# Optimization experiments

Hardware: AMD Instinct MI355X
Metric: run time of the kernel (lower is better)

The kernel has to match this reference:

```python
import jax, jax.numpy as jnp
import numpy as np
from jax import lax

# Lens/aperture geometry (must match init_kwargs lens_mask)
LENS = 21
RADIUS = LENS // 2
EPS = 1e-8


def _offsets():
    """Flattened 21x21 aperture footprint: distance kernel, circular lens mask,
    and (row, col) slice offsets into the padded image."""
    ys, xs = np.meshgrid(np.arange(LENS), np.arange(LENS), indexing='ij')
    dy = ys - RADIUS
    dx = xs - RADIUS
    dist = np.sqrt(dy * dy + dx * dx).astype(np.float32)
    mask = (dist <= RADIUS).astype(np.float32)
    return (jnp.asarray(dist.ravel()), jnp.asarray(mask.ravel()),
            jnp.asarray(ys.ravel().astype(np.int32)),
            jnp.asarray(xs.ravel().astype(np.int32)))


def scatter_layer(x5, lens_effect):
    """Scatter (splat) defocus rendering of one RGBAD layer.

    x5: [B,5,H,W] (r,g,b,alpha,relative-disparity); lens_effect: [B,1].
    Each source pixel splats its premultiplied color over a disk of radius
    r = |disp| * lens_effect (soft-edged, area-normalized). Because the disk
    kernel is symmetric in the offset, the scatter is computed as a gather
    over the 21x21 footprint with weights taken from the *source* pixel.

    Returns [B,5,H,W]: [:3] accumulated rgb, [3] accumulated weight,
    [4] occupancy (clipped accumulated alpha-weight).
    """
    B, _, H, W = x5.shape
    dist, mask, oy, ox = _offsets()
    rgb, a, disp = x5[:, :3], x5[:, 3:4], x5[:, 4:5]
    r = jnp.clip(jnp.abs(disp) * lens_effect[:, :, None, None], 0.0, float(RADIUS))  # [B,1,H,W]

    # per-source-pixel soft disk area: sum_o mask(o) * clip(r + 0.5 - dist(o), 0, 1)
    def area_step(acc, dm):
        d, m = dm
        return acc + m * jnp.clip(r + 0.5 - d, 0.0, 1.0), None

    area, _ = lax.scan(area_step, jnp.zeros_like(r), (dist, mask))

    # premultiplied source energy, normalized by splat area
    s = jnp.concatenate([rgb * a, a], axis=1) / (area + EPS)  # [B,4,H,W]
    pad = ((0, 0), (0, 0), (RADIUS, RADIUS), (RADIUS, RADIUS))
    s_pad = jnp.pad(s, pad)
    r_pad = jnp.pad(r, pad)

    # gather formulation of the scatter: out[q] = sum_o s[q-o] * w(o; r[q-o])
    def step(acc, dmyx):
        d, m, dy, dx = dmyx
        sl = lax.dynamic_slice(s_pad, (0, 0, dy, dx), (B, 4, H, W))
        rsl = lax.dynamic_slice(r_pad, (0, 0, dy, dx), (B, 1, H, W))
        w = m * jnp.clip(rsl + 0.5 - d, 0.0, 1.0)
        return acc + sl * w, None

    out4, _ = lax.scan(step, jnp.zeros((B, 4, H, W), x5.dtype), (dist, mask, oy, ox))
    occu = jnp.clip(out4[:, 3:4], 0.0, 1.0)
    return jnp.concatenate([out4, occu], axis=1)


def setup_inputs() -> dict:
    key = jax.random.key(0)
    k1, k2 = jax.random.split(key)
    B, N_LAYER, H, W = 2, 3, 512, 512
    rgbad_layers = jax.random.uniform(k1, (B, 5 * N_LAYER, H, W), dtype=jnp.float32)
    # lens strength in a range that exercises the full 21x21 footprint
    lens_effect = jax.random.uniform(k2, (B, 1), dtype=jnp.float32) * 10.0
    focal = jnp.zeros((B, 5 * N_LAYER, H, W), dtype=jnp.float32)
    return {"rgbad_layers": rgbad_layers, "lens_effect": lens_effect, "focal": focal}


def reference(rgbad_layers, lens_effect, focal):
    """Multi_Layer_Renderer.forward: front-to-back alpha compositing of
    per-layer scatter-rendered bokeh."""
    x = rgbad_layers - focal
    n_layer = x.shape[1] // 5
    blurs = [scatter_layer(x[:, 5 * i:5 * (i + 1)], lens_effect) for i in range(n_layer)]
    rgb0, w0, o0 = blurs[0][:, :3], blurs[0][:, 3:4], blurs[0][:, 4:5]
    blur_rgb = rgb0 / (w0 + EPS) * o0
    trans = 1.0 - o0  # accumulated transmittance
    for li in range(1, n_layer):
        lr, lw, lo = blurs[li][:, :3], blurs[li][:, 3:4], blurs[li][:, 4:5]
        blur_rgb = blur_rgb + lr / (lw + EPS) * (trans * lo)
        trans = trans * (1.0 - lo)
    return blur_rgb
```

## Files before the change

### kernel.cpp

```cpp
#include <hip/hip_runtime.h>
#include <hip/hip_bf16.h>

#define HH 512
#define WW 512
#define HWSZ (512*512)

typedef _Float16 hh4 __attribute__((ext_vector_type(4)));
typedef float    ff4 __attribute__((ext_vector_type(4)));

__device__ __forceinline__ float clamp01(float x) {
    return __builtin_amdgcn_fmed3f(x, 0.0f, 1.0f);
}

__global__ __launch_bounds__(256, 4)
void mlr_fused_kernel(const float* __restrict__ rgbad,
                      const float* __restrict__ lens_eff,
                      const float* __restrict__ focal,
                      float* __restrict__ out)
{
    constexpr int TW = 64, TH = 16;
    constexpr int SW = 88;
    constexpr int SH = TH + 20;
    constexpr int LP = SW + 1;
    constexpr int NG = SW / 4;
    constexpr int NSLOT = SH * NG;

    __shared__ uint2 sL[SH * LP];
    __shared__ float rL[SH * LP];
    __shared__ int   maxbits;

    const int tx  = threadIdx.x;
    const int ty  = threadIdx.y;
    const int tid = ty * 16 + tx;
    const int bx0 = blockIdx.x * TW;
    const int by0 = blockIdx.y * TH;
    const int bb  = blockIdx.z;
    const float lens = lens_eff[bb];

    static constexpr float DJ[44] = {
        0.f, 1.f, 1.41421356f, 2.f, 2.23606798f, 2.82842712f, 3.f, 3.16227766f,
        3.60555128f, 4.f, 4.12310563f, 4.24264069f, 4.47213595f, 5.f, 5.09901951f,
        5.38516481f, 5.65685425f, 5.83095189f, 6.f, 6.08276253f, 6.32455532f,
        6.40312424f, 6.70820393f, 7.f, 7.07106781f, 7.21110255f, 7.28010989f,
        7.61577311f, 7.81024968f, 8.f, 8.06225775f, 8.24621125f, 8.48528137f,
        8.54400375f, 8.60232527f, 8.94427191f, 9.f, 9.05538514f, 9.21954446f,
        9.43398113f, 9.48683298f, 9.84885780f, 9.89949494f, 10.f };
    static constexpr float CNT[44] = {
        1,4,4,4,8,4,4,8,8,4,8,4,8,12,8,8,4,8,4,8,8,8,
        8,4,12,8,8,8,8,4,16,8,4,8,8,8,4,8,16,8,8,8,4,12 };

    float blurR[4] = {0,0,0,0}, blurG[4] = {0,0,0,0}, blurB[4] = {0,0,0,0};
    float trans[4] = {1,1,1,1};

#pragma unroll 1
    for (int l = 0; l < 3; ++l) {
        __syncthreads();
        if (tid == 0) maxbits = 0;
        __syncthreads();

        const float* pin = rgbad + (size_t)(bb * 15 + 5 * l) * HWSZ;
        const float* pfo = focal + (size_t)(bb * 15 + 5 * l) * HWSZ;
        float mloc = 0.f;

#pragma unroll 1
        for (int s = tid; s < NSLOT; s += 256) {
            const int row = s / NG;
            const int grp = s - row * NG;
            const int gy  = by0 - 10 + row;
            const int gx0 = bx0 - 12 + 4 * grp;

            ff4 i0 = {0,0,0,0}, i1 = {0,0,0,0}, i2 = {0,0,0,0}, i3 = {0,0,0,0}, i4 = {0,0,0,0};
            ff4 f0 = {0,0,0,0}, f1 = {0,0,0,0}, f2 = {0,0,0,0}, f3 = {0,0,0,0}, f4 = {0,0,0,0};
            const bool valid = ((unsigned)gy < (unsigned)HH) && ((unsigned)gx0 < (unsigned)WW);
            if (valid) {
                const size_t off = (size_t)gy * WW + (size_t)gx0;
                i0 = *reinterpret_cast<const ff4*>(pin + off);
                i1 = *reinterpret_cast<const ff4*>(pin + off +   HWSZ);
                i2 = *reinterpret_cast<const ff4*>(pin + off + 2*HWSZ);
                i3 = *reinterpret_cast<const ff4*>(pin + off + 3*HWSZ);
                i4 = *reinterpret_cast<const ff4*>(pin + off + 4*HWSZ);
                f0 = *reinterpret_cast<const ff4*>(pfo + off);
                f1 = *reinterpret_cast<const ff4*>(pfo + off +   HWSZ);
                f2 = *reinterpret_cast<const ff4*>(pfo + off + 2*HWSZ);
                f3 = *reinterpret_cast<const ff4*>(pfo + off + 3*HWSZ);
                f4 = *reinterpret_cast<const ff4*>(pfo + off + 4*HWSZ);
            }
            const int base = row * LP + 4 * grp;
#pragma unroll
            for (int k = 0; k < 4; ++k) {
                const float cr = i0[k] - f0[k];
                const float cg = i1[k] - f1[k];
                const float cb = i2[k] - f2[k];
                const float ca = i3[k] - f3[k];
                const float cd = i4[k] - f4[k];
                const float r  = fminf(fabsf(cd) * lens, 10.f);
                const float rp05 = r + 0.5f;
                float a0 = 0.f, a1 = 0.f;
#pragma unroll
                for (int j = 0; j < 44; j += 2) {
                    a0 = fmaf(CNT[j],     clamp01(rp05 - DJ[j]),     a0);
                    a1 = fmaf(CNT[j + 1], clamp01(rp05 - DJ[j + 1]), a1);
                }
                const float inv = 1.0f / (a0 + a1 + 1e-8f);
                const float pa  = ca * inv;
                hh4 hv;
                hv.x = (_Float16)(cr * pa);
                hv.y = (_Float16)(cg * pa);
                hv.z = (_Float16)(cb * pa);
                hv.w = (_Float16)pa;
                sL[base + k] = __builtin_bit_cast(uint2, hv);
                rL[base + k] = rp05;
            }
            if (valid) mloc = fmaxf(mloc, fminf(fabsf(i4[0]-f4[0])*lens,10.f)+0.5f);
            if (valid) mloc = fmaxf(mloc, fminf(fabsf(i4[1]-f4[1])*lens,10.f)+0.5f);
            if (valid) mloc = fmaxf(mloc, fminf(fabsf(i4[2]-f4[2])*lens,10.f)+0.5f);
            if (valid) mloc = fmaxf(mloc, fminf(fabsf(i4[3]-f4[3])*lens,10.f)+0.5f);
        }
        atomicMax(&maxbits, __float_as_int(mloc));
        __syncthreads();

        const float rmax = __int_as_float(maxbits);
        const int U = min(10, (int)ceilf(rmax) - 1);

        float accR[4] = {0,0,0,0}, accG[4] = {0,0,0,0};
        float accB[4] = {0,0,0,0}, accW[4] = {0,0,0,0};

#define TAP(vv) { \
            const float rp = rL[rbase + (vv)]; \
            const hh4 hv = __builtin_bit_cast(hh4, sL[rbase + (vv)]); \
            const float s0 = (float)hv.x, s1 = (float)hv.y; \
            const float s2 = (float)hv.z, s3 = (float)hv.w; \
            _Pragma("unroll") \
            for (int ox = 0; ox < 4; ++ox) { \
                const int dx = (vv) - ox; \
                if (dx >= -10 && dx <= 10) { \
                    const float w = clamp01(rp - dd[dx + 10]); \
                    accR[ox] = fmaf(s0, w, accR[ox]); \
                    accG[ox] = fmaf(s1, w, accG[ox]); \
                    accB[ox] = fmaf(s2, w, accB[ox]); \
                    accW[ox] = fmaf(s3, w, accW[ox]); } } }

#pragma unroll 1
        for (int u = -U; u <= U; ++u) {
            const float u2f = (float)(u * u);
            const float vm2 = rmax * rmax - u2f;
            float dd[21];
#pragma unroll
            for (int k = 0; k < 21; ++k) {
                const int dxk = k - 10;
                const float q = u2f + (float)(dxk * dxk);
                dd[k] = (q <= 100.0f) ? __builtin_sqrtf(q) : 1e9f;
            }
            const int rbase = (ty + 10 + u) * LP + 12 + 4 * tx;

#pragma unroll
            for (int v = -2; v <= 5; ++v) TAP(v);
            if (vm2 > 9.0f) {
#pragma unroll
                for (int v = -5; v <= -3; ++v) TAP(v);
#pragma unroll
                for (int v = 6; v <= 8; ++v) TAP(v);
            }
            if (vm2 > 36.0f) {
#pragma unroll
                for (int v = -8; v <= -6; ++v) TAP(v);
#pragma unroll
                for (int v = 9; v <= 11; ++v) TAP(v);
            }
            if (vm2 > 81.0f) {
#pragma unroll
                for (int v = -10; v <= -9; ++v) TAP(v);
#pragma unroll
                for (int v = 12; v <= 13; ++v) TAP(v);
            }
        }
#undef TAP

#pragma unroll
        for (int ox = 0; ox < 4; ++ox) {
            const float wsum = accW[ox];
            const float occ  = clamp01(wsum);
            const float f    = trans[ox] * occ / (wsum + 1e-8f);
            blurR[ox] = fmaf(accR[ox], f, blurR[ox]);
            blurG[ox] = fmaf(accG[ox], f, blurG[ox]);
            blurB[ox] = fmaf(accB[ox], f, blurB[ox]);
            trans[ox] *= (1.0f - occ);
        }
    }

    const int oy = by0 + ty;
    const size_t obase = (size_t)bb * 3 * HWSZ + (size_t)oy * WW + (size_t)(bx0 + 4 * tx);

    float4 vR, vG, vB;
    vR.x = blurR[0]; vR.y = blurR[1]; vR.z = blurR[2]; vR.w = blurR[3];
    vG.x = blurG[0]; vG.y = blurG[1]; vG.z = blurG[2]; vG.w = blurG[3];
    vB.x = blurB[0]; vB.y = blurB[1]; vB.z = blurB[2]; vB.w = blurB[3];

    *reinterpret_cast<float4*>(out + obase)            = vR;
    *reinterpret_cast<float4*>(out + obase + HWSZ)     = vG;
    *reinterpret_cast<float4*>(out + obase + 2 * HWSZ) = vB;
}

extern "C" void kernel_launch(void* const* d_in, const int* in_sizes, int n_in,
                              void* d_out, int out_size, void* d_ws, size_t ws_size,
                              hipStream_t stream) {
    const float* rgbad = (const float*)d_in[0];
    const float* lens  = (const float*)d_in[1];
    const float* focal = (const float*)d_in[2];
    float* out = (float*)d_out;
    const int B = in_sizes[1];
    dim3 grid(WW / 64, HH / 16, B);
    dim3 block(16, 16, 1);
    hipLaunchKernelGGL(mlr_fused_kernel, grid, block, 0, stream,
                       rgbad, lens, focal, out);
}
```

Measured before the change: 45.83 us.

## Split gather rows across four thread slices with shared-memory reduction

Grows the block from 256 to 1024 threads by adding a z dimension. Each z slice handles every fourth row offset of the footprint, and the partial accumulators are summed serially through a shared-memory region using barriers. Staging work is also spread across 1024 threads, and the max-radius tracking now reuses the already computed rp05. This gives more parallelism per tile, at the cost of extra shared memory, extra barriers, a serial reduction, and load imbalance when U is small.

```diff
diff --git a/kernel.cpp b/kernel.cpp
--- a/kernel.cpp
+++ b/kernel.cpp
@@ -12,7 +12,7 @@
     return __builtin_amdgcn_fmed3f(x, 0.0f, 1.0f);
 }
 
-__global__ __launch_bounds__(256, 4)
+__global__ __launch_bounds__(1024)
 void mlr_fused_kernel(const float* __restrict__ rgbad,
                       const float* __restrict__ lens_eff,
                       const float* __restrict__ focal,
@@ -27,11 +27,13 @@
 
     __shared__ uint2 sL[SH * LP];
     __shared__ float rL[SH * LP];
+    __shared__ ff4  region[TH * TW];
     __shared__ int   maxbits;
 
     const int tx  = threadIdx.x;
     const int ty  = threadIdx.y;
-    const int tid = ty * 16 + tx;
+    const int tz  = threadIdx.z;
+    const int tid = tz * 256 + ty * 16 + tx;
     const int bx0 = blockIdx.x * TW;
     const int by0 = blockIdx.y * TH;
     const int bb  = blockIdx.z;
@@ -63,7 +65,7 @@
         float mloc = 0.f;
 
 #pragma unroll 1
-        for (int s = tid; s < NSLOT; s += 256) {
+        for (int s = tid; s < NSLOT; s += 1024) {
             const int row = s / NG;
             const int grp = s - row * NG;
             const int gy  = by0 - 10 + row;
@@ -110,11 +112,8 @@
                 hv.w = (_Float16)pa;
                 sL[base + k] = __builtin_bit_cast(uint2, hv);
                 rL[base + k] = rp05;
-            }
-            if (valid) mloc = fmaxf(mloc, fminf(fabsf(i4[0]-f4[0])*lens,10.f)+0.5f);
-            if (valid) mloc = fmaxf(mloc, fminf(fabsf(i4[1]-f4[1])*lens,10.f)+0.5f);
-            if (valid) mloc = fmaxf(mloc, fminf(fabsf(i4[2]-f4[2])*lens,10.f)+0.5f);
-            if (valid) mloc = fmaxf(mloc, fminf(fabsf(i4[3]-f4[3])*lens,10.f)+0.5f);
+                if (valid) mloc = fmaxf(mloc, rp05);
+            }
         }
         atomicMax(&maxbits, __float_as_int(mloc));
         __syncthreads();
@@ -141,7 +140,8 @@
                     accW[ox] = fmaf(s3, w, accW[ox]); } } }
 
 #pragma unroll 1
-        for (int u = -U; u <= U; ++u) {
+        for (int u = -10 + tz; u <= 10; u += 4) {
+            if (u < -U || u > U) continue;
             const float u2f = (float)(u * u);
             const float vm2 = rmax * rmax - u2f;
             float dd[21];
@@ -176,29 +176,62 @@
         }
 #undef TAP
 
-#pragma unroll
-        for (int ox = 0; ox < 4; ++ox) {
-            const float wsum = accW[ox];
-            const float occ  = clamp01(wsum);
-            const float f    = trans[ox] * occ / (wsum + 1e-8f);
-            blurR[ox] = fmaf(accR[ox], f, blurR[ox]);
-            blurG[ox] = fmaf(accG[ox], f, blurG[ox]);
-            blurB[ox] = fmaf(accB[ox], f, blurB[ox]);
-            trans[ox] *= (1.0f - occ);
+        const int p0 = ty * TW + 4 * tx;
+        __syncthreads();
+        if (tz == 3) {
+#pragma unroll
+            for (int ox = 0; ox < 4; ++ox) {
+                ff4 v; v.x = accR[ox]; v.y = accG[ox]; v.z = accB[ox]; v.w = accW[ox];
+                region[p0 + ox] = v;
+            }
+        }
+        __syncthreads();
+        if (tz == 2) {
+#pragma unroll
+            for (int ox = 0; ox < 4; ++ox) {
+                ff4 v = region[p0 + ox];
+                v.x += accR[ox]; v.y += accG[ox]; v.z += accB[ox]; v.w += accW[ox];
+                region[p0 + ox] = v;
+            }
+        }
+        __syncthreads();
+        if (tz == 1) {
+#pragma unroll
+            for (int ox = 0; ox < 4; ++ox) {
+                ff4 v = region[p0 + ox];
+                v.x += accR[ox]; v.y += accG[ox]; v.z += accB[ox]; v.w += accW[ox];
+                region[p0 + ox] = v;
+            }
+        }
+        __syncthreads();
+        if (tz == 0) {
+#pragma unroll
+            for (int ox = 0; ox < 4; ++ox) {
+                const ff4 v = region[p0 + ox];
+                const float wsum = accW[ox] + v.w;
+                const float occ  = clamp01(wsum);
+                const float f    = trans[ox] * occ / (wsum + 1e-8f);
+                blurR[ox] = fmaf(accR[ox] + v.x, f, blurR[ox]);
+                blurG[ox] = fmaf(accG[ox] + v.y, f, blurG[ox]);
+                blurB[ox] = fmaf(accB[ox] + v.z, f, blurB[ox]);
+                trans[ox] *= (1.0f - occ);
+            }
         }
     }
 
-    const int oy = by0 + ty;
-    const size_t obase = (size_t)bb * 3 * HWSZ + (size_t)oy * WW + (size_t)(bx0 + 4 * tx);
-
-    float4 vR, vG, vB;
-    vR.x = blurR[0]; vR.y = blurR[1]; vR.z = blurR[2]; vR.w = blurR[3];
-    vG.x = blurG[0]; vG.y = blurG[1]; vG.z = blurG[2]; vG.w = blurG[3];
-    vB.x = blurB[0]; vB.y = blurB[1]; vB.z = blurB[2]; vB.w = blurB[3];
-
-    *reinterpret_cast<float4*>(out + obase)            = vR;
-    *reinterpret_cast<float4*>(out + obase + HWSZ)     = vG;
-    *reinterpret_cast<float4*>(out + obase + 2 * HWSZ) = vB;
+    if (tz == 0) {
+        const int oy = by0 + ty;
+        const size_t obase = (size_t)bb * 3 * HWSZ + (size_t)oy * WW + (size_t)(bx0 + 4 * tx);
+
+        float4 vR, vG, vB;
+        vR.x = blurR[0]; vR.y = blurR[1]; vR.z = blurR[2]; vR.w = blurR[3];
+        vG.x = blurG[0]; vG.y = blurG[1]; vG.z = blurG[2]; vG.w = blurG[3];
+        vB.x = blurB[0]; vB.y = blurB[1]; vB.z = blurB[2]; vB.w = blurB[3];
+
+        *reinterpret_cast<float4*>(out + obase)            = vR;
+        *reinterpret_cast<float4*>(out + obase + HWSZ)     = vG;
+        *reinterpret_cast<float4*>(out + obase + 2 * HWSZ) = vB;
+    }
 }
 
 extern "C" void kernel_launch(void* const* d_in, const int* in_sizes, int n_in,
@@ -210,7 +243,7 @@
     float* out = (float*)d_out;
     const int B = in_sizes[1];
     dim3 grid(WW / 64, HH / 16, B);
-    dim3 block(16, 16, 1);
+    dim3 block(16, 16, 4);
     hipLaunchKernelGGL(mlr_fused_kernel, grid, block, 0, stream,
                        rgbad, lens, focal, out);
 }
```

After: 68.42 us. 49.3% more time.

## Pack LDS halo tile for paired 128-bit reads, fp16 radius, smaller tiles

Applied to the files above, without the earlier changes.

Shrinks the block to 16x8 threads (tile 64x8), which enlarges the relative halo overhead. Stores splat radius in fp16 packed pairs and writes source values with 128-bit LDS stores. The tap loop then reads two adjacent taps per 128-bit LDS load instead of two separate 64-bit plus 32-bit loads. The change cuts LDS instruction count and shared memory use. In exchange it adds fp16 rounding on the radius, which affects weights, and more redundant halo loading per output.

```diff
diff --git a/kernel.cpp b/kernel.cpp
--- a/kernel.cpp
+++ b/kernel.cpp
@@ -6,27 +6,28 @@
 #define HWSZ (512*512)
 
 typedef _Float16 hh4 __attribute__((ext_vector_type(4)));
+typedef _Float16 hh2 __attribute__((ext_vector_type(2)));
 typedef float    ff4 __attribute__((ext_vector_type(4)));
 
 __device__ __forceinline__ float clamp01(float x) {
     return __builtin_amdgcn_fmed3f(x, 0.0f, 1.0f);
 }
 
-__global__ __launch_bounds__(256, 4)
+__global__ __launch_bounds__(128, 3)
 void mlr_fused_kernel(const float* __restrict__ rgbad,
                       const float* __restrict__ lens_eff,
                       const float* __restrict__ focal,
                       float* __restrict__ out)
 {
-    constexpr int TW = 64, TH = 16;
+    constexpr int TW = 64, TH = 8;
     constexpr int SW = 88;
     constexpr int SH = TH + 20;
-    constexpr int LP = SW + 1;
+    constexpr int LP = 90;
     constexpr int NG = SW / 4;
     constexpr int NSLOT = SH * NG;
 
-    __shared__ uint2 sL[SH * LP];
-    __shared__ float rL[SH * LP];
+    __shared__ uint2 sP[SH * LP];
+    __shared__ uint  rP[SH * LP / 2];
     __shared__ int   maxbits;
 
     const int tx  = threadIdx.x;
@@ -63,7 +64,7 @@
         float mloc = 0.f;
 
 #pragma unroll 1
-        for (int s = tid; s < NSLOT; s += 256) {
+        for (int s = tid; s < NSLOT; s += 128) {
             const int row = s / NG;
             const int grp = s - row * NG;
             const int gy  = by0 - 10 + row;
@@ -85,7 +86,8 @@
                 f3 = *reinterpret_cast<const ff4*>(pfo + off + 3*HWSZ);
                 f4 = *reinterpret_cast<const ff4*>(pfo + off + 4*HWSZ);
             }
-            const int base = row * LP + 4 * grp;
+            uint2 pk[4];
+            unsigned short rh[4];
 #pragma unroll
             for (int k = 0; k < 4; ++k) {
                 const float cr = i0[k] - f0[k];
@@ -108,13 +110,20 @@
                 hv.y = (_Float16)(cg * pa);
                 hv.z = (_Float16)(cb * pa);
                 hv.w = (_Float16)pa;
-                sL[base + k] = __builtin_bit_cast(uint2, hv);
-                rL[base + k] = rp05;
+                pk[k] = __builtin_bit_cast(uint2, hv);
+                rh[k] = __builtin_bit_cast(unsigned short, (_Float16)rp05);
+                mloc  = fmaxf(mloc, rp05);
             }
-            if (valid) mloc = fmaxf(mloc, fminf(fabsf(i4[0]-f4[0])*lens,10.f)+0.5f);
-            if (valid) mloc = fmaxf(mloc, fminf(fabsf(i4[1]-f4[1])*lens,10.f)+0.5f);
-            if (valid) mloc = fmaxf(mloc, fminf(fabsf(i4[2]-f4[2])*lens,10.f)+0.5f);
-            if (valid) mloc = fmaxf(mloc, fminf(fabsf(i4[3]-f4[3])*lens,10.f)+0.5f);
+            const int base = row * LP + 4 * grp;
+            uint4 s01, s23;
+            s01.x = pk[0].x; s01.y = pk[0].y; s01.z = pk[1].x; s01.w = pk[1].y;
+            s23.x = pk[2].x; s23.y = pk[2].y; s23.z = pk[3].x; s23.w = pk[3].y;
+            *reinterpret_cast<uint4*>(&sP[base])     = s01;
+            *reinterpret_cast<uint4*>(&sP[base + 2]) = s23;
+            uint2 rr;
+            rr.x = (uint)rh[0] | ((uint)rh[1] << 16);
+            rr.y = (uint)rh[2] | ((uint)rh[3] << 16);
+            *reinterpret_cast<uint2*>(&rP[base >> 1]) = rr;
         }
         atomicMax(&maxbits, __float_as_int(mloc));
         __syncthreads();
@@ -125,20 +134,26 @@
         float accR[4] = {0,0,0,0}, accG[4] = {0,0,0,0};
         float accB[4] = {0,0,0,0}, accW[4] = {0,0,0,0};
 
-#define TAP(vv) { \
-            const float rp = rL[rbase + (vv)]; \
-            const hh4 hv = __builtin_bit_cast(hh4, sL[rbase + (vv)]); \
+#define TAP1(vv, sw0, sw1, rpf) { \
+            uint2 sw; sw.x = (sw0); sw.y = (sw1); \
+            const hh4 hv = __builtin_bit_cast(hh4, sw); \
             const float s0 = (float)hv.x, s1 = (float)hv.y; \
             const float s2 = (float)hv.z, s3 = (float)hv.w; \
             _Pragma("unroll") \
             for (int ox = 0; ox < 4; ++ox) { \
                 const int dx = (vv) - ox; \
                 if (dx >= -10 && dx <= 10) { \
-                    const float w = clamp01(rp - dd[dx + 10]); \
+                    const float w = clamp01((rpf) - dd[dx + 10]); \
                     accR[ox] = fmaf(s0, w, accR[ox]); \
                     accG[ox] = fmaf(s1, w, accG[ox]); \
                     accB[ox] = fmaf(s2, w, accB[ox]); \
                     accW[ox] = fmaf(s3, w, accW[ox]); } } }
+
+#define PAIR(v0) { \
+            const uint4 sp = *reinterpret_cast<const uint4*>(&sP[rbase + (v0)]); \
+            const hh2 rp2 = __builtin_bit_cast(hh2, rP[(rbase + (v0)) >> 1]); \
+            TAP1((v0),     sp.x, sp.y, (float)rp2.x); \
+            TAP1((v0) + 1, sp.z, sp.w, (float)rp2.y); }
 
 #pragma unroll 1
         for (int u = -U; u <= U; ++u) {
@@ -153,28 +168,13 @@
             }
             const int rbase = (ty + 10 + u) * LP + 12 + 4 * tx;
 
-#pragma unroll
-            for (int v = -2; v <= 5; ++v) TAP(v);
-            if (vm2 > 9.0f) {
-#pragma unroll
-                for (int v = -5; v <= -3; ++v) TAP(v);
-#pragma unroll
-                for (int v = 6; v <= 8; ++v) TAP(v);
-            }
-            if (vm2 > 36.0f) {
-#pragma unroll
-                for (int v = -8; v <= -6; ++v) TAP(v);
-#pragma unroll
-                for (int v = 9; v <= 11; ++v) TAP(v);
-            }
-            if (vm2 > 81.0f) {
-#pragma unroll
-                for (int v = -10; v <= -9; ++v) TAP(v);
-#pragma unroll
-                for (int v = 12; v <= 13; ++v) TAP(v);
-            }
+            PAIR(-2) PAIR(0) PAIR(2) PAIR(4)
+            if (vm2 > 9.0f)  { PAIR(-6) PAIR(-4) PAIR(6) PAIR(8) }
+            if (vm2 > 36.0f) { PAIR(-8) PAIR(10) }
+            if (vm2 > 81.0f) { PAIR(-10) PAIR(12) }
         }
-#undef TAP
+#undef PAIR
+#undef TAP1
 
 #pragma unroll
         for (int ox = 0; ox < 4; ++ox) {
@@ -209,8 +209,8 @@
     const float* focal = (const float*)d_in[2];
     float* out = (float*)d_out;
     const int B = in_sizes[1];
-    dim3 grid(WW / 64, HH / 16, B);
-    dim3 block(16, 16, 1);
+    dim3 grid(WW / 64, HH / 8, B);
+    dim3 block(16, 8, 1);
     hipLaunchKernelGGL(mlr_fused_kernel, grid, block, 0, stream,
                        rgbad, lens, focal, out);
 }
```

Result: slower. 54.29 us (+18.5%).
